# Kernel tuning notes

Measured on AMD Instinct MI355X. Metric: run time of the kernel, lower is better.

The kernel has to match this reference:

```python
import jax, jax.numpy as jnp
import numpy as np

N_NODES = 100000
N_EDGES = 1200000
NUM_GRAPHS = 128
IN_DIM = 5
HIDDEN = 64


def setup_inputs() -> dict:
    key = jax.random.key(0)
    ks = jax.random.split(key, 12)
    x = jax.random.normal(ks[0], (N_NODES, IN_DIM), dtype=jnp.float32)
    edge_index = jax.random.randint(ks[1], (2, N_EDGES), 0, N_NODES, dtype=jnp.int64 if jax.config.read('jax_enable_x64') else jnp.int32)
    batch = jnp.sort(jax.random.randint(ks[2], (N_NODES,), 0, NUM_GRAPHS, dtype=jnp.int32))
    s = lambda fan_in: 1.0 / np.sqrt(fan_in)
    return {
        'x': x,
        'edge_index': edge_index,
        'batch': batch,
        'w_rel1': jax.random.normal(ks[3], (IN_DIM, HIDDEN), dtype=jnp.float32) * s(IN_DIM),
        'b_rel1': jnp.zeros((HIDDEN,), dtype=jnp.float32),
        'w_root1': jax.random.normal(ks[4], (IN_DIM, HIDDEN), dtype=jnp.float32) * s(IN_DIM),
        'w_rel2': jax.random.normal(ks[5], (HIDDEN, HIDDEN), dtype=jnp.float32) * s(HIDDEN),
        'b_rel2': jnp.zeros((HIDDEN,), dtype=jnp.float32),
        'w_root2': jax.random.normal(ks[6], (HIDDEN, HIDDEN), dtype=jnp.float32) * s(HIDDEN),
        'w_h1': jax.random.normal(ks[7], (2 * HIDDEN, HIDDEN), dtype=jnp.float32) * s(2 * HIDDEN),
        'b_h1': jnp.zeros((HIDDEN,), dtype=jnp.float32),
        'w_h2': jax.random.normal(ks[8], (HIDDEN, 1), dtype=jnp.float32) * s(HIDDEN),
        'b_h2': jnp.zeros((1,), dtype=jnp.float32),
    }


def _graph_conv(x, src, dst, w_rel, b_rel, w_root):
    # PyG GraphConv (aggr='add'): out = aggr(x_src -> dst) @ W_rel + b_rel + x @ W_root
    agg = jax.ops.segment_sum(x[src], dst, num_segments=N_NODES)
    return agg @ w_rel + b_rel + x @ w_root


def reference(x, edge_index, batch,
              w_rel1, b_rel1, w_root1,
              w_rel2, b_rel2, w_root2,
              w_h1, b_h1, w_h2, b_h2):
    src, dst = edge_index[0], edge_index[1]
    h = jax.nn.relu(_graph_conv(x, src, dst, w_rel1, b_rel1, w_root1))
    h = jax.nn.relu(_graph_conv(h, src, dst, w_rel2, b_rel2, w_root2))
    # global add + mean pooling over graphs
    add_pool = jax.ops.segment_sum(h, batch, num_segments=NUM_GRAPHS)
    counts = jax.ops.segment_sum(jnp.ones((N_NODES,), h.dtype), batch, num_segments=NUM_GRAPHS)
    mean_pool = add_pool / jnp.maximum(counts, 1.0)[:, None]
    g = jnp.concatenate([mean_pool, add_pool], axis=1)  # [G, 2*HIDDEN]
    out = jax.nn.relu(g @ w_h1 + b_h1) @ w_h2 + b_h2
    return out.squeeze(-1)
```

## Files before the change

kernel.cpp:

```cpp
#include <hip/hip_runtime.h>
#include <hip/hip_bf16.h>

#define N_NODES    100000
#define N_EDGES    1200000
#define NUM_GRAPHS 128
#define IN_DIM     5
#define HIDDEN     64
#define M_TILES    (N_NODES / 16)
#define NI4        (N_EDGES / 4)

#define CB    782
#define CBLK  256
#define EPB   ((NI4 + CBLK - 1) / CBLK)

typedef __attribute__((ext_vector_type(8))) short short8;
typedef __attribute__((ext_vector_type(4))) float f32x4;

__device__ __forceinline__ int rfl(int v) { return __builtin_amdgcn_readfirstlane(v); }

__device__ __forceinline__ unsigned short f2bs(float f) {
    union { float f; unsigned u; } v; v.f = f;
    return (unsigned short)((v.u + 0x7FFFu + ((v.u >> 16) & 1u)) >> 16);
}
__device__ __forceinline__ float bs2f(unsigned short s) {
    union { unsigned u; float f; } v; v.u = ((unsigned)s) << 16;
    return v.f;
}
__device__ __forceinline__ float blo(unsigned p) { return bs2f((unsigned short)(p & 0xffff)); }
__device__ __forceinline__ float bhi(unsigned p) { return bs2f((unsigned short)(p >> 16)); }
__device__ __forceinline__ unsigned pack2(float a, float b) {
    return ((unsigned)f2bs(b) << 16) | (unsigned)f2bs(a);
}

__device__ __forceinline__ unsigned char f2f8(float f) {
    union { float f; unsigned u; } v; v.f = f * 0x1p-120f;
    unsigned u = v.u + 0x7FFFFu + ((v.u >> 20) & 1u);
    return (unsigned char)(u >> 20);
}
__device__ __forceinline__ float f82f(unsigned b) {
    union { unsigned u; float f; } v; v.u = (b & 0x7Fu) << 20;
    return v.f * 0x1p120f;
}


__global__ void coarse_count(const int* __restrict__ dst, int* __restrict__ gcnt,
                             const float* __restrict__ x, uint4* __restrict__ xb) {
    __shared__ int h[CB];
    int t = threadIdx.x, b = blockIdx.x;
    for (int i = t; i < CB; i += 256) h[i] = 0;
    __syncthreads();
    int i0 = b * EPB, i1 = min(i0 + EPB, NI4);
    for (int i = i0 + t; i < i1; i += 256) {
        int4 d = ((const int4*)dst)[i];
        atomicAdd(&h[d.x >> 7], 1);
        atomicAdd(&h[d.y >> 7], 1);
        atomicAdd(&h[d.z >> 7], 1);
        atomicAdd(&h[d.w >> 7], 1);
    }
    __syncthreads();
    for (int i = t; i < CB; i += 256) gcnt[b * CB + i] = h[i];

    for (int n = b * 256 + t; n < N_NODES; n += CBLK * 256) {
        const float* xr = x + (size_t)n * IN_DIM;
        uint4 o;
        o.x = pack2(xr[0], xr[1]);
        o.y = pack2(xr[2], xr[3]);
        o.z = pack2(xr[4], 0.0f);
        o.w = 0u;
        xb[n] = o;
    }
}

__global__ void block_scan(int* __restrict__ gcnt, int* __restrict__ btot) {
    __shared__ int s[CBLK];
    int k = blockIdx.x, t = threadIdx.x;
    int v = gcnt[t * CB + k];
    s[t] = v;
    __syncthreads();
    for (int off = 1; off < CBLK; off <<= 1) {
        int x = (t >= off) ? s[t - off] : 0;
        __syncthreads();
        s[t] += x;
        __syncthreads();
    }
    gcnt[t * CB + k] = s[t] - v;
    if (t == CBLK - 1) btot[k] = s[t];
}

__global__ void bucket_scan(const int* __restrict__ btot, int* __restrict__ bstart,
                            float* __restrict__ add_pool) {
    __shared__ int s[1024];
    int t = threadIdx.x;
    int v = (t < CB) ? btot[t] : 0;
    s[t] = v;
    __syncthreads();
    for (int off = 1; off < 1024; off <<= 1) {
        int x = (t >= off) ? s[t - off] : 0;
        __syncthreads();
        s[t] += x;
        __syncthreads();
    }
    if (t < CB) bstart[t] = s[t] - v;
    if (t == 0) bstart[CB] = N_EDGES;
    for (int i = t; i < NUM_GRAPHS * HIDDEN; i += 1024) add_pool[i] = 0.0f;
}

__global__ void partition_k(const int* __restrict__ src, const int* __restrict__ dst,
                            const int* __restrict__ gcnt, const int* __restrict__ bstart,
                            int* __restrict__ part) {
    __shared__ int base[CB];
    __shared__ int h[CB];
    int t = threadIdx.x, b = blockIdx.x;
    for (int i = t; i < CB; i += 256) {
        base[i] = bstart[i] + gcnt[b * CB + i];
        h[i] = 0;
    }
    __syncthreads();
    int i0 = b * EPB, i1 = min(i0 + EPB, NI4);
    for (int i = i0 + t; i < i1; i += 256) {
        int4 s4 = ((const int4*)src)[i];
        int4 d4 = ((const int4*)dst)[i];
        int k, r;
        k = d4.x >> 7; r = atomicAdd(&h[k], 1); part[base[k] + r] = s4.x | ((d4.x & 127) << 17);
        k = d4.y >> 7; r = atomicAdd(&h[k], 1); part[base[k] + r] = s4.y | ((d4.y & 127) << 17);
        k = d4.z >> 7; r = atomicAdd(&h[k], 1); part[base[k] + r] = s4.z | ((d4.z & 127) << 17);
        k = d4.w >> 7; r = atomicAdd(&h[k], 1); part[base[k] + r] = s4.w | ((d4.w & 127) << 17);
    }
}

__global__ void fine_sort(const int* __restrict__ part, const int* __restrict__ bstart,
                          int* __restrict__ ptr, int* __restrict__ esrc) {
    __shared__ int fh[128];
    __shared__ int fr[128];
    int k = blockIdx.x, t = threadIdx.x;
    int e0 = bstart[k], e1 = bstart[k + 1];
    if (t < 128) { fh[t] = 0; fr[t] = 0; }
    __syncthreads();
    for (int e = e0 + t; e < e1; e += 256)
        atomicAdd(&fh[(part[e] >> 17) & 127], 1);
    __syncthreads();
    if (t == 0) {
        int run = 0;
        for (int i = 0; i < 128; ++i) { int c = fh[i]; fh[i] = run; run += c; }
    }
    __syncthreads();
    int n0 = k << 7;
    if (t < 128 && n0 + t < N_NODES) ptr[n0 + t] = e0 + fh[t];
    for (int e = e0 + t; e < e1; e += 256) {
        int p = part[e];
        int d = (p >> 17) & 127;
        int r = atomicAdd(&fr[d], 1);
        esrc[e0 + fh[d] + r] = p & 0x1FFFF;
    }
}


__global__ void gather_mlp1(const uint4* __restrict__ xb,
                            const float* __restrict__ x,
                            const int* __restrict__ ptr,
                            const int* __restrict__ esrc,
                            const float* __restrict__ w_rel1,
                            const float* __restrict__ b_rel1,
                            const float* __restrict__ w_root1,
                            unsigned short* __restrict__ h1,
                            unsigned char* __restrict__ h1f8) {
    int lane = threadIdx.x & 63;
    int w    = (blockIdx.x * blockDim.x + threadIdx.x) >> 6;
    int nw   = (gridDim.x * blockDim.x) >> 6;

    float wr[IN_DIM], wo[IN_DIM];
#pragma unroll
    for (int k = 0; k < IN_DIM; ++k) {
        wr[k] = w_rel1[k * HIDDEN + lane];
        wo[k] = w_root1[k * HIDDEN + lane];
    }
    float bias = b_rel1[lane];

    for (int n = w; n < N_NODES; n += nw) {
        int start = rfl(ptr[n]);
        int end   = rfl((n + 1 < N_NODES) ? ptr[n + 1] : N_EDGES);
        float a[IN_DIM] = {0.f, 0.f, 0.f, 0.f, 0.f};
        for (int e = start + lane; e < end; e += 64) {
            uint4 p = xb[esrc[e]];
            a[0] += blo(p.x); a[1] += bhi(p.x);
            a[2] += blo(p.y); a[3] += bhi(p.y);
            a[4] += blo(p.z);
        }
#pragma unroll
        for (int k = 0; k < IN_DIM; ++k)
#pragma unroll
            for (int off = 1; off < 64; off <<= 1)
                a[k] += __shfl_xor(a[k], off, 64);
        float acc = bias;
#pragma unroll
        for (int k = 0; k < IN_DIM; ++k)
            acc += a[k] * wr[k] + x[(size_t)n * IN_DIM + k] * wo[k];
        float hv = fmaxf(acc, 0.0f);
        h1[(size_t)n * HIDDEN + lane]   = f2bs(hv);
        h1f8[(size_t)n * HIDDEN + lane] = f2f8(hv);
    }
}

__global__ void gather2_fp8(const unsigned* __restrict__ h1f8,
                            const int* __restrict__ ptr,
                            const int* __restrict__ esrc,
                            uint2* __restrict__ agg2) {
    int lane = threadIdx.x & 63;
    int ql   = lane & 15;
    int q    = lane >> 4;
    int w    = (blockIdx.x * blockDim.x + threadIdx.x) >> 6;
    int nw   = (gridDim.x * blockDim.x) >> 6;

    for (int n = w; n < N_NODES; n += nw) {
        int start = rfl(ptr[n]);
        int end   = rfl((n + 1 < N_NODES) ? ptr[n + 1] : N_EDGES);
        float4 a0 = {0.f,0.f,0.f,0.f}, a1 = a0, a2 = a0, a3 = a0;
        int e = start + q;
        for (; e + 12 < end; e += 16) {
            int s0 = esrc[e], s1 = esrc[e + 4], s2 = esrc[e + 8], s3 = esrc[e + 12];
            unsigned p0 = h1f8[(size_t)s0 * 16 + ql];
            unsigned p1 = h1f8[(size_t)s1 * 16 + ql];
            unsigned p2 = h1f8[(size_t)s2 * 16 + ql];
            unsigned p3 = h1f8[(size_t)s3 * 16 + ql];
            a0.x += f82f(p0); a0.y += f82f(p0 >> 8); a0.z += f82f(p0 >> 16); a0.w += f82f(p0 >> 24);
            a1.x += f82f(p1); a1.y += f82f(p1 >> 8); a1.z += f82f(p1 >> 16); a1.w += f82f(p1 >> 24);
            a2.x += f82f(p2); a2.y += f82f(p2 >> 8); a2.z += f82f(p2 >> 16); a2.w += f82f(p2 >> 24);
            a3.x += f82f(p3); a3.y += f82f(p3 >> 8); a3.z += f82f(p3 >> 16); a3.w += f82f(p3 >> 24);
        }
        for (; e < end; e += 4) {
            unsigned p = h1f8[(size_t)esrc[e] * 16 + ql];
            a0.x += f82f(p); a0.y += f82f(p >> 8); a0.z += f82f(p >> 16); a0.w += f82f(p >> 24);
        }
        float4 a;
        a.x = (a0.x + a1.x) + (a2.x + a3.x);
        a.y = (a0.y + a1.y) + (a2.y + a3.y);
        a.z = (a0.z + a1.z) + (a2.z + a3.z);
        a.w = (a0.w + a1.w) + (a2.w + a3.w);
        a.x += __shfl_xor(a.x, 16, 64); a.x += __shfl_xor(a.x, 32, 64);
        a.y += __shfl_xor(a.y, 16, 64); a.y += __shfl_xor(a.y, 32, 64);
        a.z += __shfl_xor(a.z, 16, 64); a.z += __shfl_xor(a.z, 32, 64);
        a.w += __shfl_xor(a.w, 16, 64); a.w += __shfl_xor(a.w, 32, 64);
        if (q == 0) {
            uint2 o;
            o.x = pack2(a.x, a.y);
            o.y = pack2(a.z, a.w);
            agg2[(size_t)n * 16 + ql] = o;
        }
    }
}

__global__ void mlp2_pool(const unsigned short* __restrict__ agg2,
                          const unsigned short* __restrict__ h1,
                          const float* __restrict__ w_rel2,
                          const float* __restrict__ b_rel2,
                          const float* __restrict__ w_root2,
                          const int* __restrict__ batch,
                          float* __restrict__ add_pool) {
    int lane = threadIdx.x & 63;
    int wv   = threadIdx.x >> 6;
    int row  = lane & 15;
    int quad = lane >> 4;
    int n    = wv * 16 + row;

    short8 bwr[2], bwo[2];
#pragma unroll
    for (int s = 0; s < 2; ++s)
#pragma unroll
        for (int j = 0; j < 8; ++j) {
            int k = 32 * s + quad * 8 + j;
            bwr[s][j] = (short)f2bs(w_rel2[k * HIDDEN + n]);
            bwo[s][j] = (short)f2bs(w_root2[k * HIDDEN + n]);
        }
    float bias = b_rel2[n];

    for (int t = blockIdx.x; t < M_TILES; t += gridDim.x) {
        int m0 = t * 16;
        size_t rbase = (size_t)(m0 + row) * HIDDEN;
        short8 aa0 = *(const short8*)(agg2 + rbase + quad * 8);
        short8 aa1 = *(const short8*)(agg2 + rbase + 32 + quad * 8);
        short8 ah0 = *(const short8*)(h1   + rbase + quad * 8);
        short8 ah1 = *(const short8*)(h1   + rbase + 32 + quad * 8);

        f32x4 acc = {bias, bias, bias, bias};
        acc = __builtin_amdgcn_mfma_f32_16x16x32_bf16(aa0, bwr[0], acc, 0, 0, 0);
        acc = __builtin_amdgcn_mfma_f32_16x16x32_bf16(aa1, bwr[1], acc, 0, 0, 0);
        acc = __builtin_amdgcn_mfma_f32_16x16x32_bf16(ah0, bwo[0], acc, 0, 0, 0);
        acc = __builtin_amdgcn_mfma_f32_16x16x32_bf16(ah1, bwo[1], acc, 0, 0, 0);

        float hv0 = fmaxf(acc[0], 0.0f), hv1 = fmaxf(acc[1], 0.0f);
        float hv2 = fmaxf(acc[2], 0.0f), hv3 = fmaxf(acc[3], 0.0f);

        int gLo = batch[m0], gHi = batch[m0 + 15];
        if (gLo == gHi) {
            float s = (hv0 + hv1) + (hv2 + hv3);
            s += __shfl_xor(s, 16, 64);
            s += __shfl_xor(s, 32, 64);
            if (quad == 0)
                atomicAdd(&add_pool[gLo * HIDDEN + n], s);
        } else {
            int m = m0 + quad * 4;
            atomicAdd(&add_pool[batch[m]     * HIDDEN + n], hv0);
            atomicAdd(&add_pool[batch[m + 1] * HIDDEN + n], hv1);
            atomicAdd(&add_pool[batch[m + 2] * HIDDEN + n], hv2);
            atomicAdd(&add_pool[batch[m + 3] * HIDDEN + n], hv3);
        }
    }
}

__device__ __forceinline__ int lower_bound_i(const int* a, int n, int v) {
    int lo = 0, hi = n;
    while (lo < hi) { int mid = (lo + hi) >> 1; if (a[mid] < v) lo = mid + 1; else hi = mid; }
    return lo;
}

__global__ void head_mlp(const float* __restrict__ add_pool,
                         const int* __restrict__ batch,
                         const float* __restrict__ w_h1,
                         const float* __restrict__ b_h1,
                         const float* __restrict__ w_h2,
                         const float* __restrict__ b_h2,
                         float* __restrict__ out) {
    int g = blockIdx.x, t = threadIdx.x;

    __shared__ int s_cnt;
    if (t == 0) {
        int start = lower_bound_i(batch, N_NODES, g);
        int end   = lower_bound_i(batch, N_NODES, g + 1);
        s_cnt = end - start;
    }
    __syncthreads();
    float cnt = fmaxf((float)s_cnt, 1.0f);

    __shared__ float sg[2 * HIDDEN];
    float add = add_pool[(size_t)g * HIDDEN + t];
    sg[t]          = add / cnt;
    sg[HIDDEN + t] = add;
    __syncthreads();

    float hid = b_h1[t];
#pragma unroll 16
    for (int i = 0; i < 2 * HIDDEN; ++i)
        hid += sg[i] * w_h1[i * HIDDEN + t];
    hid = fmaxf(hid, 0.0f);

    float res = hid * w_h2[t];
    for (int off = 32; off > 0; off >>= 1)
        res += __shfl_down(res, off, 64);
    if (t == 0) out[g] = res + b_h2[0];
}

extern "C" void kernel_launch(void* const* d_in, const int* in_sizes, int n_in,
                              void* d_out, int out_size, void* d_ws, size_t ws_size,
                              hipStream_t stream) {
    const float* x       = (const float*)d_in[0];
    const int*   ei      = (const int*)d_in[1];
    const int*   src     = ei;
    const int*   dst     = ei + N_EDGES;
    const int*   batch   = (const int*)d_in[2];
    const float* w_rel1  = (const float*)d_in[3];
    const float* b_rel1  = (const float*)d_in[4];
    const float* w_root1 = (const float*)d_in[5];
    const float* w_rel2  = (const float*)d_in[6];
    const float* b_rel2  = (const float*)d_in[7];
    const float* w_root2 = (const float*)d_in[8];
    const float* w_h1    = (const float*)d_in[9];
    const float* b_h1    = (const float*)d_in[10];
    const float* w_h2    = (const float*)d_in[11];
    const float* b_h2    = (const float*)d_in[12];
    float* out = (float*)d_out;

    int* base = (int*)d_ws;
    int*   gcnt     = base;
    int*   btot     = gcnt + ((CBLK * CB + 3) & ~3);
    int*   bstart   = btot + ((CB + 3) & ~3);
    float* add_pool = (float*)(bstart + ((CB + 1 + 3) & ~3));
    int*   ptr      = (int*)(add_pool + NUM_GRAPHS * HIDDEN);
    int*   part     = ptr + ((N_NODES + 3) & ~3);
    int*   esrc     = part + N_EDGES;
    unsigned short* h1   = (unsigned short*)(esrc + N_EDGES);
    unsigned short* agg2 = h1 + (size_t)N_NODES * HIDDEN;
    unsigned char*  h1f8 = (unsigned char*)(agg2 + (size_t)N_NODES * HIDDEN);
    uint4*          xb   = (uint4*)(h1f8 + (size_t)N_NODES * HIDDEN);

    coarse_count<<<CBLK, 256, 0, stream>>>(dst, gcnt, x, xb);
    block_scan<<<CB, CBLK, 0, stream>>>(gcnt, btot);
    bucket_scan<<<1, 1024, 0, stream>>>(btot, bstart, add_pool);
    partition_k<<<CBLK, 256, 0, stream>>>(src, dst, gcnt, bstart, part);
    fine_sort<<<CB, 256, 0, stream>>>(part, bstart, ptr, esrc);

    gather_mlp1<<<2048, 256, 0, stream>>>(xb, x, ptr, esrc, w_rel1, b_rel1, w_root1, h1, h1f8);
    gather2_fp8<<<2048, 256, 0, stream>>>((const unsigned*)h1f8, ptr, esrc, (uint2*)agg2);
    mlp2_pool<<<2048, 256, 0, stream>>>(agg2, h1, w_rel2, b_rel2, w_root2, batch, add_pool);
    head_mlp<<<NUM_GRAPHS, 64, 0, stream>>>(add_pool, batch, w_h1, b_h1, w_h2, b_h2, out);
}
```

Before: 229.9 us.

## Drop fine sort; aggregate per coarse bucket with LDS float atomics

Removes the fine_sort kernel and the CSR ptr/esrc arrays. Both aggregation layers now work directly on coarse 128-node buckets, accumulating into shared memory with float atomicAdd and then applying the layer-1 MLP or writing packed bf16 agg2. This saves one kernel launch and a full pass over the edge list, at the cost of LDS atomic contention and non-deterministic summation order.

```diff
diff --git a/kernel.cpp b/kernel.cpp
--- a/kernel.cpp
+++ b/kernel.cpp
@@ -12,11 +12,10 @@
 #define CB    782
 #define CBLK  256
 #define EPB   ((NI4 + CBLK - 1) / CBLK)
+#define ST2   65
 
 typedef __attribute__((ext_vector_type(8))) short short8;
 typedef __attribute__((ext_vector_type(4))) float f32x4;
-
-__device__ __forceinline__ int rfl(int v) { return __builtin_amdgcn_readfirstlane(v); }
 
 __device__ __forceinline__ unsigned short f2bs(float f) {
     union { float f; unsigned u; } v; v.f = f;
@@ -128,124 +127,103 @@
     }
 }
 
-__global__ void fine_sort(const int* __restrict__ part, const int* __restrict__ bstart,
-                          int* __restrict__ ptr, int* __restrict__ esrc) {
-    __shared__ int fh[128];
-    __shared__ int fr[128];
+
+__global__ void l1_bucket(const uint4* __restrict__ xb,
+                          const float* __restrict__ x,
+                          const int* __restrict__ part,
+                          const int* __restrict__ bstart,
+                          const float* __restrict__ w_rel1,
+                          const float* __restrict__ b_rel1,
+                          const float* __restrict__ w_root1,
+                          unsigned short* __restrict__ h1,
+                          unsigned char* __restrict__ h1f8) {
+    __shared__ float sa[128 * IN_DIM];
     int k = blockIdx.x, t = threadIdx.x;
+    for (int i = t; i < 128 * IN_DIM; i += 256) sa[i] = 0.0f;
+    __syncthreads();
+
     int e0 = bstart[k], e1 = bstart[k + 1];
-    if (t < 128) { fh[t] = 0; fr[t] = 0; }
-    __syncthreads();
-    for (int e = e0 + t; e < e1; e += 256)
-        atomicAdd(&fh[(part[e] >> 17) & 127], 1);
-    __syncthreads();
-    if (t == 0) {
-        int run = 0;
-        for (int i = 0; i < 128; ++i) { int c = fh[i]; fh[i] = run; run += c; }
-    }
-    __syncthreads();
-    int n0 = k << 7;
-    if (t < 128 && n0 + t < N_NODES) ptr[n0 + t] = e0 + fh[t];
     for (int e = e0 + t; e < e1; e += 256) {
-        int p = part[e];
-        int d = (p >> 17) & 127;
-        int r = atomicAdd(&fr[d], 1);
-        esrc[e0 + fh[d] + r] = p & 0x1FFFF;
-    }
-}
-
-
-__global__ void gather_mlp1(const uint4* __restrict__ xb,
-                            const float* __restrict__ x,
-                            const int* __restrict__ ptr,
-                            const int* __restrict__ esrc,
-                            const float* __restrict__ w_rel1,
-                            const float* __restrict__ b_rel1,
-                            const float* __restrict__ w_root1,
-                            unsigned short* __restrict__ h1,
-                            unsigned char* __restrict__ h1f8) {
-    int lane = threadIdx.x & 63;
-    int w    = (blockIdx.x * blockDim.x + threadIdx.x) >> 6;
-    int nw   = (gridDim.x * blockDim.x) >> 6;
-
+        unsigned p = (unsigned)part[e];
+        uint4 xv = xb[p & 0x1FFFFu];
+        float* ac = sa + ((p >> 17) & 127u) * IN_DIM;
+        atomicAdd(ac + 0, blo(xv.x));
+        atomicAdd(ac + 1, bhi(xv.x));
+        atomicAdd(ac + 2, blo(xv.y));
+        atomicAdd(ac + 3, bhi(xv.y));
+        atomicAdd(ac + 4, blo(xv.z));
+    }
+    __syncthreads();
+
+    int ch = t & 63;
     float wr[IN_DIM], wo[IN_DIM];
 #pragma unroll
-    for (int k = 0; k < IN_DIM; ++k) {
-        wr[k] = w_rel1[k * HIDDEN + lane];
-        wo[k] = w_root1[k * HIDDEN + lane];
-    }
-    float bias = b_rel1[lane];
-
-    for (int n = w; n < N_NODES; n += nw) {
-        int start = rfl(ptr[n]);
-        int end   = rfl((n + 1 < N_NODES) ? ptr[n + 1] : N_EDGES);
-        float a[IN_DIM] = {0.f, 0.f, 0.f, 0.f, 0.f};
-        for (int e = start + lane; e < end; e += 64) {
-            uint4 p = xb[esrc[e]];
-            a[0] += blo(p.x); a[1] += bhi(p.x);
-            a[2] += blo(p.y); a[3] += bhi(p.y);
-            a[4] += blo(p.z);
-        }
-#pragma unroll
-        for (int k = 0; k < IN_DIM; ++k)
-#pragma unroll
-            for (int off = 1; off < 64; off <<= 1)
-                a[k] += __shfl_xor(a[k], off, 64);
+    for (int kk = 0; kk < IN_DIM; ++kk) {
+        wr[kk] = w_rel1[kk * HIDDEN + ch];
+        wo[kk] = w_root1[kk * HIDDEN + ch];
+    }
+    float bias = b_rel1[ch];
+    int n0 = k << 7;
+    for (int nl = t >> 6; nl < 128; nl += 4) {
+        int n = n0 + nl;
+        if (n >= N_NODES) break;
         float acc = bias;
 #pragma unroll
-        for (int k = 0; k < IN_DIM; ++k)
-            acc += a[k] * wr[k] + x[(size_t)n * IN_DIM + k] * wo[k];
+        for (int kk = 0; kk < IN_DIM; ++kk)
+            acc += sa[nl * IN_DIM + kk] * wr[kk] + x[(size_t)n * IN_DIM + kk] * wo[kk];
         float hv = fmaxf(acc, 0.0f);
-        h1[(size_t)n * HIDDEN + lane]   = f2bs(hv);
-        h1f8[(size_t)n * HIDDEN + lane] = f2f8(hv);
-    }
-}
-
-__global__ void gather2_fp8(const unsigned* __restrict__ h1f8,
-                            const int* __restrict__ ptr,
-                            const int* __restrict__ esrc,
-                            uint2* __restrict__ agg2) {
-    int lane = threadIdx.x & 63;
-    int ql   = lane & 15;
-    int q    = lane >> 4;
-    int w    = (blockIdx.x * blockDim.x + threadIdx.x) >> 6;
-    int nw   = (gridDim.x * blockDim.x) >> 6;
-
-    for (int n = w; n < N_NODES; n += nw) {
-        int start = rfl(ptr[n]);
-        int end   = rfl((n + 1 < N_NODES) ? ptr[n + 1] : N_EDGES);
-        float4 a0 = {0.f,0.f,0.f,0.f}, a1 = a0, a2 = a0, a3 = a0;
-        int e = start + q;
-        for (; e + 12 < end; e += 16) {
-            int s0 = esrc[e], s1 = esrc[e + 4], s2 = esrc[e + 8], s3 = esrc[e + 12];
-            unsigned p0 = h1f8[(size_t)s0 * 16 + ql];
-            unsigned p1 = h1f8[(size_t)s1 * 16 + ql];
-            unsigned p2 = h1f8[(size_t)s2 * 16 + ql];
-            unsigned p3 = h1f8[(size_t)s3 * 16 + ql];
-            a0.x += f82f(p0); a0.y += f82f(p0 >> 8); a0.z += f82f(p0 >> 16); a0.w += f82f(p0 >> 24);
-            a1.x += f82f(p1); a1.y += f82f(p1 >> 8); a1.z += f82f(p1 >> 16); a1.w += f82f(p1 >> 24);
-            a2.x += f82f(p2); a2.y += f82f(p2 >> 8); a2.z += f82f(p2 >> 16); a2.w += f82f(p2 >> 24);
-            a3.x += f82f(p3); a3.y += f82f(p3 >> 8); a3.z += f82f(p3 >> 16); a3.w += f82f(p3 >> 24);
-        }
-        for (; e < end; e += 4) {
-            unsigned p = h1f8[(size_t)esrc[e] * 16 + ql];
-            a0.x += f82f(p); a0.y += f82f(p >> 8); a0.z += f82f(p >> 16); a0.w += f82f(p >> 24);
-        }
-        float4 a;
-        a.x = (a0.x + a1.x) + (a2.x + a3.x);
-        a.y = (a0.y + a1.y) + (a2.y + a3.y);
-        a.z = (a0.z + a1.z) + (a2.z + a3.z);
-        a.w = (a0.w + a1.w) + (a2.w + a3.w);
-        a.x += __shfl_xor(a.x, 16, 64); a.x += __shfl_xor(a.x, 32, 64);
-        a.y += __shfl_xor(a.y, 16, 64); a.y += __shfl_xor(a.y, 32, 64);
-        a.z += __shfl_xor(a.z, 16, 64); a.z += __shfl_xor(a.z, 32, 64);
-        a.w += __shfl_xor(a.w, 16, 64); a.w += __shfl_xor(a.w, 32, 64);
-        if (q == 0) {
-            uint2 o;
-            o.x = pack2(a.x, a.y);
-            o.y = pack2(a.z, a.w);
-            agg2[(size_t)n * 16 + ql] = o;
-        }
+        h1[(size_t)n * HIDDEN + ch]   = f2bs(hv);
+        h1f8[(size_t)n * HIDDEN + ch] = f2f8(hv);
+    }
+}
+
+__global__ void l2_bucket(const unsigned* __restrict__ h1f8r,
+                          const int* __restrict__ part,
+                          const int* __restrict__ bstart,
+                          unsigned* __restrict__ agg2u) {
+    __shared__ float sa[128 * ST2];
+    int k = blockIdx.x, t = threadIdx.x;
+    int g = t >> 4, ql = t & 15;
+    for (int i = t; i < 128 * ST2; i += 256) sa[i] = 0.0f;
+    __syncthreads();
+
+    int e0 = bstart[k], e1 = bstart[k + 1];
+    int e = e0 + g;
+    for (; e + 16 < e1; e += 32) {
+        unsigned pa = (unsigned)part[e];
+        unsigned pb = (unsigned)part[e + 16];
+        unsigned ra = h1f8r[(size_t)(pa & 0x1FFFFu) * 16 + ql];
+        unsigned rb = h1f8r[(size_t)(pb & 0x1FFFFu) * 16 + ql];
+        float* aa = sa + ((pa >> 17) & 127u) * ST2 + ql * 4;
+        float* ab = sa + ((pb >> 17) & 127u) * ST2 + ql * 4;
+        atomicAdd(aa + 0, f82f(ra));
+        atomicAdd(aa + 1, f82f(ra >> 8));
+        atomicAdd(aa + 2, f82f(ra >> 16));
+        atomicAdd(aa + 3, f82f(ra >> 24));
+        atomicAdd(ab + 0, f82f(rb));
+        atomicAdd(ab + 1, f82f(rb >> 8));
+        atomicAdd(ab + 2, f82f(rb >> 16));
+        atomicAdd(ab + 3, f82f(rb >> 24));
+    }
+    if (e < e1) {
+        unsigned p = (unsigned)part[e];
+        unsigned r = h1f8r[(size_t)(p & 0x1FFFFu) * 16 + ql];
+        float* ac = sa + ((p >> 17) & 127u) * ST2 + ql * 4;
+        atomicAdd(ac + 0, f82f(r));
+        atomicAdd(ac + 1, f82f(r >> 8));
+        atomicAdd(ac + 2, f82f(r >> 16));
+        atomicAdd(ac + 3, f82f(r >> 24));
+    }
+    __syncthreads();
+
+    int n0 = k << 7;
+    int cp = t & 31;
+    for (int nl = t >> 5; nl < 128; nl += 8) {
+        int n = n0 + nl;
+        if (n >= N_NODES) break;
+        float c0 = sa[nl * ST2 + cp * 2];
+        float c1 = sa[nl * ST2 + cp * 2 + 1];
+        agg2u[(size_t)n * 32 + cp] = pack2(c0, c1);
     }
 }
 
@@ -374,10 +352,8 @@
     int*   btot     = gcnt + ((CBLK * CB + 3) & ~3);
     int*   bstart   = btot + ((CB + 3) & ~3);
     float* add_pool = (float*)(bstart + ((CB + 1 + 3) & ~3));
-    int*   ptr      = (int*)(add_pool + NUM_GRAPHS * HIDDEN);
-    int*   part     = ptr + ((N_NODES + 3) & ~3);
-    int*   esrc     = part + N_EDGES;
-    unsigned short* h1   = (unsigned short*)(esrc + N_EDGES);
+    int*   part     = (int*)(add_pool + NUM_GRAPHS * HIDDEN);
+    unsigned short* h1   = (unsigned short*)(part + N_EDGES);
     unsigned short* agg2 = h1 + (size_t)N_NODES * HIDDEN;
     unsigned char*  h1f8 = (unsigned char*)(agg2 + (size_t)N_NODES * HIDDEN);
     uint4*          xb   = (uint4*)(h1f8 + (size_t)N_NODES * HIDDEN);
@@ -386,10 +362,9 @@
     block_scan<<<CB, CBLK, 0, stream>>>(gcnt, btot);
     bucket_scan<<<1, 1024, 0, stream>>>(btot, bstart, add_pool);
     partition_k<<<CBLK, 256, 0, stream>>>(src, dst, gcnt, bstart, part);
-    fine_sort<<<CB, 256, 0, stream>>>(part, bstart, ptr, esrc);
-
-    gather_mlp1<<<2048, 256, 0, stream>>>(xb, x, ptr, esrc, w_rel1, b_rel1, w_root1, h1, h1f8);
-    gather2_fp8<<<2048, 256, 0, stream>>>((const unsigned*)h1f8, ptr, esrc, (uint2*)agg2);
+
+    l1_bucket<<<CB, 256, 0, stream>>>(xb, x, part, bstart, w_rel1, b_rel1, w_root1, h1, h1f8);
+    l2_bucket<<<CB, 256, 0, stream>>>((const unsigned*)h1f8, part, bstart, (unsigned*)agg2);
     mlp2_pool<<<2048, 256, 0, stream>>>(agg2, h1, w_rel2, b_rel2, w_root2, batch, add_pool);
     head_mlp<<<NUM_GRAPHS, 64, 0, stream>>>(add_pool, batch, w_h1, b_h1, w_h2, b_h2, out);
 }
```

Measured after the change: 694.9 us. +202.3%, slower.

## Replace two-level bucket sort CSR build with global-atomic degree count and scatter

Applied to the files above, without the earlier changes.

Builds the CSR with per-node global atomics: zero the degrees, count them atomically, run a single-block chunked scan into ptr and cur, then scatter sources through atomic cursors. This drops the two-level coarse/fine bucket sort with its intermediate part buffer and several launches. Both gather kernels now assign 16 lanes per node instead of a full wave, which cuts shuffle reductions and idle lanes for low-degree nodes. In exchange it relies on contended global atomics, edge order within a node becomes nondeterministic, and the single-block serial scan over 100k degrees may be slow.

```diff
diff --git a/kernel.cpp b/kernel.cpp
--- a/kernel.cpp
+++ b/kernel.cpp
@@ -9,14 +9,12 @@
 #define M_TILES    (N_NODES / 16)
 #define NI4        (N_EDGES / 4)
 
-#define CB    782
 #define CBLK  256
 #define EPB   ((NI4 + CBLK - 1) / CBLK)
+#define SCAN_CH 98
 
 typedef __attribute__((ext_vector_type(8))) short short8;
 typedef __attribute__((ext_vector_type(4))) float f32x4;
-
-__device__ __forceinline__ int rfl(int v) { return __builtin_amdgcn_readfirstlane(v); }
 
 __device__ __forceinline__ unsigned short f2bs(float f) {
     union { float f; unsigned u; } v; v.f = f;
@@ -43,23 +41,22 @@
 }
 
 
-__global__ void coarse_count(const int* __restrict__ dst, int* __restrict__ gcnt,
-                             const float* __restrict__ x, uint4* __restrict__ xb) {
-    __shared__ int h[CB];
+__global__ void zero_k(int* __restrict__ deg) {
+    int i = blockIdx.x * blockDim.x + threadIdx.x;
+    if (i <= N_NODES) deg[i] = 0;
+}
+
+__global__ void deg_xb(const int* __restrict__ dst, int* __restrict__ deg,
+                       const float* __restrict__ x, uint4* __restrict__ xb) {
     int t = threadIdx.x, b = blockIdx.x;
-    for (int i = t; i < CB; i += 256) h[i] = 0;
-    __syncthreads();
     int i0 = b * EPB, i1 = min(i0 + EPB, NI4);
     for (int i = i0 + t; i < i1; i += 256) {
         int4 d = ((const int4*)dst)[i];
-        atomicAdd(&h[d.x >> 7], 1);
-        atomicAdd(&h[d.y >> 7], 1);
-        atomicAdd(&h[d.z >> 7], 1);
-        atomicAdd(&h[d.w >> 7], 1);
-    }
-    __syncthreads();
-    for (int i = t; i < CB; i += 256) gcnt[b * CB + i] = h[i];
-
+        atomicAdd(&deg[d.x], 1);
+        atomicAdd(&deg[d.y], 1);
+        atomicAdd(&deg[d.z], 1);
+        atomicAdd(&deg[d.w], 1);
+    }
     for (int n = b * 256 + t; n < N_NODES; n += CBLK * 256) {
         const float* xr = x + (size_t)n * IN_DIM;
         uint4 o;
@@ -71,86 +68,49 @@
     }
 }
 
-__global__ void block_scan(int* __restrict__ gcnt, int* __restrict__ btot) {
-    __shared__ int s[CBLK];
-    int k = blockIdx.x, t = threadIdx.x;
-    int v = gcnt[t * CB + k];
-    s[t] = v;
-    __syncthreads();
-    for (int off = 1; off < CBLK; off <<= 1) {
-        int x = (t >= off) ? s[t - off] : 0;
-        __syncthreads();
-        s[t] += x;
-        __syncthreads();
-    }
-    gcnt[t * CB + k] = s[t] - v;
-    if (t == CBLK - 1) btot[k] = s[t];
-}
-
-__global__ void bucket_scan(const int* __restrict__ btot, int* __restrict__ bstart,
-                            float* __restrict__ add_pool) {
+__global__ void scan_ptr(const int* __restrict__ deg, int* __restrict__ ptr,
+                         int* __restrict__ cur, float* __restrict__ add_pool) {
     __shared__ int s[1024];
     int t = threadIdx.x;
-    int v = (t < CB) ? btot[t] : 0;
-    s[t] = v;
+    int base = t * SCAN_CH;
+    int sum = 0;
+    for (int j = 0; j < SCAN_CH; ++j) {
+        int idx = base + j;
+        if (idx < N_NODES) sum += deg[idx];
+    }
+    s[t] = sum;
     __syncthreads();
     for (int off = 1; off < 1024; off <<= 1) {
-        int x = (t >= off) ? s[t - off] : 0;
+        int v = (t >= off) ? s[t - off] : 0;
         __syncthreads();
-        s[t] += x;
+        s[t] += v;
         __syncthreads();
     }
-    if (t < CB) bstart[t] = s[t] - v;
-    if (t == 0) bstart[CB] = N_EDGES;
+    int running = s[t] - sum;
+    for (int j = 0; j < SCAN_CH; ++j) {
+        int idx = base + j;
+        if (idx < N_NODES) {
+            ptr[idx] = running;
+            cur[idx] = running;
+            running += deg[idx];
+        }
+    }
+    if (t == 1023) ptr[N_NODES] = N_EDGES;
     for (int i = t; i < NUM_GRAPHS * HIDDEN; i += 1024) add_pool[i] = 0.0f;
 }
 
-__global__ void partition_k(const int* __restrict__ src, const int* __restrict__ dst,
-                            const int* __restrict__ gcnt, const int* __restrict__ bstart,
-                            int* __restrict__ part) {
-    __shared__ int base[CB];
-    __shared__ int h[CB];
+__global__ void scatter_k(const int* __restrict__ src, const int* __restrict__ dst,
+                          int* __restrict__ cur, int* __restrict__ esrc) {
     int t = threadIdx.x, b = blockIdx.x;
-    for (int i = t; i < CB; i += 256) {
-        base[i] = bstart[i] + gcnt[b * CB + i];
-        h[i] = 0;
-    }
-    __syncthreads();
     int i0 = b * EPB, i1 = min(i0 + EPB, NI4);
     for (int i = i0 + t; i < i1; i += 256) {
         int4 s4 = ((const int4*)src)[i];
         int4 d4 = ((const int4*)dst)[i];
-        int k, r;
-        k = d4.x >> 7; r = atomicAdd(&h[k], 1); part[base[k] + r] = s4.x | ((d4.x & 127) << 17);
-        k = d4.y >> 7; r = atomicAdd(&h[k], 1); part[base[k] + r] = s4.y | ((d4.y & 127) << 17);
-        k = d4.z >> 7; r = atomicAdd(&h[k], 1); part[base[k] + r] = s4.z | ((d4.z & 127) << 17);
-        k = d4.w >> 7; r = atomicAdd(&h[k], 1); part[base[k] + r] = s4.w | ((d4.w & 127) << 17);
-    }
-}
-
-__global__ void fine_sort(const int* __restrict__ part, const int* __restrict__ bstart,
-                          int* __restrict__ ptr, int* __restrict__ esrc) {
-    __shared__ int fh[128];
-    __shared__ int fr[128];
-    int k = blockIdx.x, t = threadIdx.x;
-    int e0 = bstart[k], e1 = bstart[k + 1];
-    if (t < 128) { fh[t] = 0; fr[t] = 0; }
-    __syncthreads();
-    for (int e = e0 + t; e < e1; e += 256)
-        atomicAdd(&fh[(part[e] >> 17) & 127], 1);
-    __syncthreads();
-    if (t == 0) {
-        int run = 0;
-        for (int i = 0; i < 128; ++i) { int c = fh[i]; fh[i] = run; run += c; }
-    }
-    __syncthreads();
-    int n0 = k << 7;
-    if (t < 128 && n0 + t < N_NODES) ptr[n0 + t] = e0 + fh[t];
-    for (int e = e0 + t; e < e1; e += 256) {
-        int p = part[e];
-        int d = (p >> 17) & 127;
-        int r = atomicAdd(&fr[d], 1);
-        esrc[e0 + fh[d] + r] = p & 0x1FFFF;
+        int r;
+        r = atomicAdd(&cur[d4.x], 1); esrc[r] = s4.x;
+        r = atomicAdd(&cur[d4.y], 1); esrc[r] = s4.y;
+        r = atomicAdd(&cur[d4.z], 1); esrc[r] = s4.z;
+        r = atomicAdd(&cur[d4.w], 1); esrc[r] = s4.w;
     }
 }
 
@@ -164,88 +124,92 @@
                             const float* __restrict__ w_root1,
                             unsigned short* __restrict__ h1,
                             unsigned char* __restrict__ h1f8) {
-    int lane = threadIdx.x & 63;
-    int w    = (blockIdx.x * blockDim.x + threadIdx.x) >> 6;
-    int nw   = (gridDim.x * blockDim.x) >> 6;
-
-    float wr[IN_DIM], wo[IN_DIM];
-#pragma unroll
-    for (int k = 0; k < IN_DIM; ++k) {
-        wr[k] = w_rel1[k * HIDDEN + lane];
-        wo[k] = w_root1[k * HIDDEN + lane];
-    }
-    float bias = b_rel1[lane];
-
-    for (int n = w; n < N_NODES; n += nw) {
-        int start = rfl(ptr[n]);
-        int end   = rfl((n + 1 < N_NODES) ? ptr[n + 1] : N_EDGES);
+    int t    = threadIdx.x;
+    int ql   = t & 15;
+    int grp  = (blockIdx.x * blockDim.x + t) >> 4;
+    int ngrp = (gridDim.x * blockDim.x) >> 4;
+
+    float wr[IN_DIM][4], wo[IN_DIM][4], bias[4];
+#pragma unroll
+    for (int j = 0; j < 4; ++j) {
+        int ch = ql * 4 + j;
+        bias[j] = b_rel1[ch];
+#pragma unroll
+        for (int k = 0; k < IN_DIM; ++k) {
+            wr[k][j] = w_rel1[k * HIDDEN + ch];
+            wo[k][j] = w_root1[k * HIDDEN + ch];
+        }
+    }
+
+    for (int n = grp; n < N_NODES; n += ngrp) {
+        int start = ptr[n], end = ptr[n + 1];
         float a[IN_DIM] = {0.f, 0.f, 0.f, 0.f, 0.f};
-        for (int e = start + lane; e < end; e += 64) {
+        for (int e = start + ql; e < end; e += 16) {
             uint4 p = xb[esrc[e]];
             a[0] += blo(p.x); a[1] += bhi(p.x);
             a[2] += blo(p.y); a[3] += bhi(p.y);
             a[4] += blo(p.z);
         }
 #pragma unroll
-        for (int k = 0; k < IN_DIM; ++k)
-#pragma unroll
-            for (int off = 1; off < 64; off <<= 1)
-                a[k] += __shfl_xor(a[k], off, 64);
-        float acc = bias;
-#pragma unroll
-        for (int k = 0; k < IN_DIM; ++k)
-            acc += a[k] * wr[k] + x[(size_t)n * IN_DIM + k] * wo[k];
-        float hv = fmaxf(acc, 0.0f);
-        h1[(size_t)n * HIDDEN + lane]   = f2bs(hv);
-        h1f8[(size_t)n * HIDDEN + lane] = f2f8(hv);
-    }
-}
-
-__global__ void gather2_fp8(const unsigned* __restrict__ h1f8,
+        for (int k = 0; k < IN_DIM; ++k) {
+            a[k] += __shfl_xor(a[k], 1, 64);
+            a[k] += __shfl_xor(a[k], 2, 64);
+            a[k] += __shfl_xor(a[k], 4, 64);
+            a[k] += __shfl_xor(a[k], 8, 64);
+        }
+        float xr[IN_DIM];
+#pragma unroll
+        for (int k = 0; k < IN_DIM; ++k) xr[k] = x[(size_t)n * IN_DIM + k];
+
+        unsigned short hv[4];
+        unsigned char  hf[4];
+#pragma unroll
+        for (int j = 0; j < 4; ++j) {
+            float acc = bias[j];
+#pragma unroll
+            for (int k = 0; k < IN_DIM; ++k)
+                acc += a[k] * wr[k][j] + xr[k] * wo[k][j];
+            float h = fmaxf(acc, 0.0f);
+            hv[j] = f2bs(h);
+            hf[j] = f2f8(h);
+        }
+        ushort4 v4; v4.x = hv[0]; v4.y = hv[1]; v4.z = hv[2]; v4.w = hv[3];
+        *(ushort4*)(h1 + (size_t)n * HIDDEN + ql * 4) = v4;
+        uchar4 c4; c4.x = hf[0]; c4.y = hf[1]; c4.z = hf[2]; c4.w = hf[3];
+        *(uchar4*)(h1f8 + (size_t)n * HIDDEN + ql * 4) = c4;
+    }
+}
+
+__global__ void gather2_fp8(const unsigned* __restrict__ rows,
                             const int* __restrict__ ptr,
                             const int* __restrict__ esrc,
                             uint2* __restrict__ agg2) {
-    int lane = threadIdx.x & 63;
-    int ql   = lane & 15;
-    int q    = lane >> 4;
-    int w    = (blockIdx.x * blockDim.x + threadIdx.x) >> 6;
-    int nw   = (gridDim.x * blockDim.x) >> 6;
-
-    for (int n = w; n < N_NODES; n += nw) {
-        int start = rfl(ptr[n]);
-        int end   = rfl((n + 1 < N_NODES) ? ptr[n + 1] : N_EDGES);
-        float4 a0 = {0.f,0.f,0.f,0.f}, a1 = a0, a2 = a0, a3 = a0;
-        int e = start + q;
-        for (; e + 12 < end; e += 16) {
-            int s0 = esrc[e], s1 = esrc[e + 4], s2 = esrc[e + 8], s3 = esrc[e + 12];
-            unsigned p0 = h1f8[(size_t)s0 * 16 + ql];
-            unsigned p1 = h1f8[(size_t)s1 * 16 + ql];
-            unsigned p2 = h1f8[(size_t)s2 * 16 + ql];
-            unsigned p3 = h1f8[(size_t)s3 * 16 + ql];
-            a0.x += f82f(p0); a0.y += f82f(p0 >> 8); a0.z += f82f(p0 >> 16); a0.w += f82f(p0 >> 24);
-            a1.x += f82f(p1); a1.y += f82f(p1 >> 8); a1.z += f82f(p1 >> 16); a1.w += f82f(p1 >> 24);
-            a2.x += f82f(p2); a2.y += f82f(p2 >> 8); a2.z += f82f(p2 >> 16); a2.w += f82f(p2 >> 24);
-            a3.x += f82f(p3); a3.y += f82f(p3 >> 8); a3.z += f82f(p3 >> 16); a3.w += f82f(p3 >> 24);
-        }
-        for (; e < end; e += 4) {
-            unsigned p = h1f8[(size_t)esrc[e] * 16 + ql];
-            a0.x += f82f(p); a0.y += f82f(p >> 8); a0.z += f82f(p >> 16); a0.w += f82f(p >> 24);
-        }
-        float4 a;
-        a.x = (a0.x + a1.x) + (a2.x + a3.x);
-        a.y = (a0.y + a1.y) + (a2.y + a3.y);
-        a.z = (a0.z + a1.z) + (a2.z + a3.z);
-        a.w = (a0.w + a1.w) + (a2.w + a3.w);
-        a.x += __shfl_xor(a.x, 16, 64); a.x += __shfl_xor(a.x, 32, 64);
-        a.y += __shfl_xor(a.y, 16, 64); a.y += __shfl_xor(a.y, 32, 64);
-        a.z += __shfl_xor(a.z, 16, 64); a.z += __shfl_xor(a.z, 32, 64);
-        a.w += __shfl_xor(a.w, 16, 64); a.w += __shfl_xor(a.w, 32, 64);
-        if (q == 0) {
-            uint2 o;
-            o.x = pack2(a.x, a.y);
-            o.y = pack2(a.z, a.w);
-            agg2[(size_t)n * 16 + ql] = o;
-        }
+    int t    = threadIdx.x;
+    int ql   = t & 15;
+    int grp  = (blockIdx.x * blockDim.x + t) >> 4;
+    int ngrp = (gridDim.x * blockDim.x) >> 4;
+
+    for (int n = grp; n < N_NODES; n += ngrp) {
+        int start = ptr[n], end = ptr[n + 1];
+        float4 a = {0.f, 0.f, 0.f, 0.f};
+        float4 b = {0.f, 0.f, 0.f, 0.f};
+        int e = start;
+        for (; e + 1 < end; e += 2) {
+            int s0 = esrc[e], s1 = esrc[e + 1];
+            unsigned r0 = rows[(size_t)s0 * 16 + ql];
+            unsigned r1 = rows[(size_t)s1 * 16 + ql];
+            a.x += f82f(r0); a.y += f82f(r0 >> 8); a.z += f82f(r0 >> 16); a.w += f82f(r0 >> 24);
+            b.x += f82f(r1); b.y += f82f(r1 >> 8); b.z += f82f(r1 >> 16); b.w += f82f(r1 >> 24);
+        }
+        if (e < end) {
+            unsigned r0 = rows[(size_t)esrc[e] * 16 + ql];
+            a.x += f82f(r0); a.y += f82f(r0 >> 8); a.z += f82f(r0 >> 16); a.w += f82f(r0 >> 24);
+        }
+        a.x += b.x; a.y += b.y; a.z += b.z; a.w += b.w;
+        uint2 o;
+        o.x = pack2(a.x, a.y);
+        o.y = pack2(a.z, a.w);
+        agg2[(size_t)n * 16 + ql] = o;
     }
 }
 
@@ -370,23 +334,20 @@
     float* out = (float*)d_out;
 
     int* base = (int*)d_ws;
-    int*   gcnt     = base;
-    int*   btot     = gcnt + ((CBLK * CB + 3) & ~3);
-    int*   bstart   = btot + ((CB + 3) & ~3);
-    float* add_pool = (float*)(bstart + ((CB + 1 + 3) & ~3));
-    int*   ptr      = (int*)(add_pool + NUM_GRAPHS * HIDDEN);
-    int*   part     = ptr + ((N_NODES + 3) & ~3);
-    int*   esrc     = part + N_EDGES;
+    int*   deg      = base;
+    int*   ptr      = deg + ((N_NODES + 1 + 3) & ~3);
+    int*   cur      = ptr + ((N_NODES + 1 + 3) & ~3);
+    float* add_pool = (float*)(cur + ((N_NODES + 3) & ~3));
+    int*   esrc     = (int*)(add_pool + NUM_GRAPHS * HIDDEN);
     unsigned short* h1   = (unsigned short*)(esrc + N_EDGES);
     unsigned short* agg2 = h1 + (size_t)N_NODES * HIDDEN;
     unsigned char*  h1f8 = (unsigned char*)(agg2 + (size_t)N_NODES * HIDDEN);
     uint4*          xb   = (uint4*)(h1f8 + (size_t)N_NODES * HIDDEN);
 
-    coarse_count<<<CBLK, 256, 0, stream>>>(dst, gcnt, x, xb);
-    block_scan<<<CB, CBLK, 0, stream>>>(gcnt, btot);
-    bucket_scan<<<1, 1024, 0, stream>>>(btot, bstart, add_pool);
-    partition_k<<<CBLK, 256, 0, stream>>>(src, dst, gcnt, bstart, part);
-    fine_sort<<<CB, 256, 0, stream>>>(part, bstart, ptr, esrc);
+    zero_k<<<(N_NODES + 1 + 1023) / 1024, 1024, 0, stream>>>(deg);
+    deg_xb<<<CBLK, 256, 0, stream>>>(dst, deg, x, xb);
+    scan_ptr<<<1, 1024, 0, stream>>>(deg, ptr, cur, add_pool);
+    scatter_k<<<CBLK, 256, 0, stream>>>(src, dst, cur, esrc);
 
     gather_mlp1<<<2048, 256, 0, stream>>>(xb, x, ptr, esrc, w_rel1, b_rel1, w_root1, h1, h1f8);
     gather2_fp8<<<2048, 256, 0, stream>>>((const unsigned*)h1f8, ptr, esrc, (uint2*)agg2);
```

New measurement: 553.2 us. +140.7%, slower.
